# Optimization experiments

Hardware: AMD Instinct MI355X
Metric: run time of the kernel (lower is better)

## Reference

```python
import jax, jax.numpy as jnp
import numpy as np

BETA = 0.8
THR = 1.0  # snntorch Leaky default threshold


def _heaviside(x):
    return (x > 0).astype(x.dtype)


def setup_inputs() -> dict:
    key = jax.random.key(0)
    ks = jax.random.split(key, 8)
    B, T, F, H, L, O = 256, 512, 8, 256, 4, 8
    x = jax.random.normal(ks[0], (B, T, F), dtype=jnp.float32)
    hidden_states = jnp.zeros((B, T, L, H), dtype=jnp.float32)
    prev_obs = jnp.zeros((B, T, F), dtype=jnp.float32)
    readout_states = jnp.zeros((B, T, O), dtype=jnp.float32)
    # fc1: Linear(8, H)
    W1 = jax.random.normal(ks[1], (F, H), dtype=jnp.float32) / np.sqrt(F)
    b1 = jnp.zeros((H,), dtype=jnp.float32)
    # hidden linears: L-1 of [H,H]; final linear [H,O]
    Wh = jax.random.normal(ks[2], (L - 1, H, H), dtype=jnp.float32) / np.sqrt(H)
    bh = jnp.zeros((L - 1, H), dtype=jnp.float32)
    Wout = jax.random.normal(ks[3], (H, O), dtype=jnp.float32) / np.sqrt(H)
    bout = jnp.zeros((O,), dtype=jnp.float32)
    return {"x": x, "hidden_states": hidden_states, "prev_obs": prev_obs,
            "readout_states": readout_states, "W1": W1, "b1": b1,
            "Wh": Wh, "bh": bh, "Wout": Wout, "bout": bout}


def reference(x, hidden_states, prev_obs, readout_states, W1, b1, Wh, bh, Wout, bout):
    # x: [B,T,F]; hidden_states: [B,T,L,H]; readout_states: [B,T,O]
    L = Wh.shape[0] + 1
    mem0 = hidden_states[:, 0]          # [B,L,H]
    ro0 = readout_states[:, 0]          # [B,O]
    # fc1 applied to all timesteps at once (as in the original)
    all_cur = jnp.einsum('btf,fh->bth', x, W1) + b1  # [B,T,H]

    def step(carry, cur_t):
        mem, ro = carry                 # mem: [B,L,H], ro: [B,O]
        cur = cur_t                     # [B,H]
        for i in range(L):
            m = mem[:, i]
            # snntorch Leaky (reset_mechanism='subtract'):
            # reset computed from previous mem, detached
            reset = _heaviside(m - THR)
            m = BETA * m + cur - reset * THR
            spk = _heaviside(m - THR)
            mem = mem.at[:, i].set(m)
            if i < L - 1:
                cur = spk @ Wh[i] + bh[i]
            else:
                cur = spk @ Wout + bout  # [B,O]
        # readout Leaky with reset_mechanism='none'
        ro = BETA * ro + cur
        return (mem, ro), (ro, mem)

    (_, _), (ros, mems) = jax.lax.scan(step, (mem0, ro0), jnp.swapaxes(all_cur, 0, 1))
    outputs = jnp.swapaxes(ros, 0, 1)            # [B,T,O]
    new_hidden_states = jnp.swapaxes(mems, 0, 1)  # [B,T,L,H]
    new_prev_obs = x
    new_readout_states = outputs
    return outputs, new_hidden_states, new_prev_obs, new_readout_states
```

## Files before the change

kernel.cpp:

```cpp
#include <hip/hip_runtime.h>

#define BB   256
#define TT   512
#define FF   8
#define HH   256
#define LL   4
#define OO   8
#define BETA 0.8f
#define THRV 1.0f

#define OFF_OUT  0
#define OFF_HID  (BB*TT*OO)
#define OFF_PREV (OFF_HID + (size_t)BB*TT*LL*HH)
#define OFF_RO   (OFF_PREV + BB*TT*FF)

typedef float nf4 __attribute__((ext_vector_type(4)));

__launch_bounds__(512, 1)
__global__ void snn_kernel(const float* __restrict__ x,
                           const float* __restrict__ hidden_in,
                           const float* __restrict__ readout_in,
                           const float* __restrict__ W1,
                           const float* __restrict__ b1,
                           const float* __restrict__ Wh,
                           const float* __restrict__ bh,
                           const float* __restrict__ Wout,
                           const float* __restrict__ bout,
                           float* __restrict__ out)
{
    __shared__ int   s_list[HH];
    __shared__ int   s_wcnt[4];
    __shared__ float s_part[HH];
    __shared__ float s_rop[4 * OO];

    const int tid  = threadIdx.x;
    const int b    = blockIdx.x;
    const int h    = tid & (HH - 1);
    const int half = tid >> 8;
    const int lane = tid & 63;
    const int wave = tid >> 6;

    {
        const nf4* xs = (const nf4*)(x + (size_t)b * TT * FF);
        nf4*       po = (nf4*)(out + OFF_PREV + (size_t)b * TT * FF);
        #pragma unroll
        for (int i = 0; i < (TT * FF / 4) / 512; ++i)
            __builtin_nontemporal_store(xs[tid + i * 512], po + tid + i * 512);
    }

    float m[LL] = {0, 0, 0, 0};
    float w1c[FF];
    float b1c = 0, bhc0 = 0, bhc1 = 0, bhc2 = 0;
    float wo[OO];
    #pragma unroll
    for (int o = 0; o < OO; ++o) wo[o] = 0.0f;
    if (half == 0) {
        const size_t hb = (size_t)b * TT * LL * HH;
        #pragma unroll
        for (int i = 0; i < LL; ++i) m[i] = hidden_in[hb + i * HH + h];
        #pragma unroll
        for (int f = 0; f < FF; ++f) w1c[f] = W1[f * HH + h];
        b1c  = b1[h];
        bhc0 = bh[0 * HH + h]; bhc1 = bh[1 * HH + h]; bhc2 = bh[2 * HH + h];
        #pragma unroll
        for (int o = 0; o < OO; ++o) wo[o] = Wout[h * OO + o];
    }
    float ro = 0, boutc = 0;
    if (tid < OO) { ro = readout_in[(size_t)b * TT * OO + tid]; boutc = bout[tid]; }

    const float* xb     = x + (size_t)b * TT * FF;
    float* hid_out      = out + OFF_HID + (size_t)b * TT * LL * HH;
    float* out_o        = out + OFF_OUT + (size_t)b * TT * OO;
    float* out_r        = out + OFF_RO  + (size_t)b * TT * OO;

    for (int t = 0; t < TT; ++t) {
        float* hrow = hid_out + (size_t)t * LL * HH;
        float c = 0.0f;
        if (half == 0) {
            c = b1c;
            #pragma unroll
            for (int f = 0; f < FF; ++f) c += xb[t * FF + f] * w1c[f];
        }

        #pragma unroll
        for (int i = 0; i < 3; ++i) {
            int spk = 0;
            unsigned long long bmask = 0ull;
            if (half == 0) {
                float mm = m[i];
                float reset = (mm > THRV) ? THRV : 0.0f;
                mm = BETA * mm + c - reset;
                spk = (mm > THRV) ? 1 : 0;
                m[i] = mm;
                __builtin_nontemporal_store(mm, hrow + i * HH + h);
                bmask = __ballot(spk);
                if (lane == 0) s_wcnt[wave] = __popcll(bmask);
            }
            __syncthreads();
            const int n0 = s_wcnt[0], n1 = s_wcnt[1], n2 = s_wcnt[2], n3 = s_wcnt[3];
            const int n = n0 + n1 + n2 + n3;
            if (half == 0 && spk) {
                int base = (wave > 0 ? n0 : 0) + (wave > 1 ? n1 : 0) + (wave > 2 ? n2 : 0);
                int pos = base + __popcll(bmask & ((1ull << lane) - 1ull));
                s_list[pos] = h << 8;
            }
            __syncthreads();

            const float* Wb = Wh + i * (HH * HH) + h;
            float cc = (half == 0) ? (i == 0 ? bhc0 : (i == 1 ? bhc1 : bhc2)) : 0.0f;
            int j = half;
            while (j + 14 < n) {
                int a0 = s_list[j],      a1 = s_list[j + 2];
                int a2 = s_list[j + 4],  a3 = s_list[j + 6];
                int a4 = s_list[j + 8],  a5 = s_list[j + 10];
                int a6 = s_list[j + 12], a7 = s_list[j + 14];
                float w0 = Wb[a0], w1 = Wb[a1], w2 = Wb[a2], w3 = Wb[a3];
                float w4 = Wb[a4], w5 = Wb[a5], w6 = Wb[a6], w7 = Wb[a7];
                cc += ((w0 + w1) + (w2 + w3)) + ((w4 + w5) + (w6 + w7));
                j += 16;
            }
            while (j < n) { cc += Wb[s_list[j]]; j += 2; }

            if (half == 1) s_part[h] = cc;
            __syncthreads();
            if (half == 0) c = cc + s_part[h];
        }

        if (half == 0) {
            float mm = m[3];
            float reset = (mm > THRV) ? THRV : 0.0f;
            mm = BETA * mm + c - reset;
            int spk3 = (mm > THRV) ? 1 : 0;
            m[3] = mm;
            __builtin_nontemporal_store(mm, hrow + 3 * HH + h);

            float s = spk3 ? 1.0f : 0.0f;
            float c8[OO];
            #pragma unroll
            for (int o = 0; o < OO; ++o) c8[o] = s * wo[o];
            #pragma unroll
            for (int d = 1; d < 64; d <<= 1) {
                #pragma unroll
                for (int o = 0; o < OO; ++o) c8[o] += __shfl_xor(c8[o], d);
            }
            if (lane == 0) {
                #pragma unroll
                for (int o = 0; o < OO; ++o) s_rop[wave * OO + o] = c8[o];
            }
        }
        __syncthreads();
        if (tid < OO) {
            float s = boutc + s_rop[tid] + s_rop[OO + tid] + s_rop[2 * OO + tid] + s_rop[3 * OO + tid];
            ro = BETA * ro + s;
            __builtin_nontemporal_store(ro, out_o + t * OO + tid);
            __builtin_nontemporal_store(ro, out_r + t * OO + tid);
        }
    }
}

extern "C" void kernel_launch(void* const* d_in, const int* in_sizes, int n_in,
                              void* d_out, int out_size, void* d_ws, size_t ws_size,
                              hipStream_t stream) {
    const float* x       = (const float*)d_in[0];
    const float* hidden  = (const float*)d_in[1];
    const float* readout = (const float*)d_in[3];
    const float* W1      = (const float*)d_in[4];
    const float* b1      = (const float*)d_in[5];
    const float* Wh      = (const float*)d_in[6];
    const float* bh      = (const float*)d_in[7];
    const float* Wout    = (const float*)d_in[8];
    const float* bout    = (const float*)d_in[9];
    float* out = (float*)d_out;

    snn_kernel<<<dim3(BB), dim3(512), 0, stream>>>(
        x, hidden, readout, W1, b1, Wh, bh, Wout, bout, out);
}
```

Measured before the change: 2.257 ms.

## Restructure SNN step to cut barriers with atomic spike lists and readout wave

Each layer's spike list is now built with one per-wave atomicAdd into a triple-buffered shared list, replacing the count-then-prefix pass. This reduces the barriers per timestep from about ten to four. The second half of the block, which split the sparse gather, is dropped. A fifth wave computes the Wout readout from the previous step's spike mask, overlapping it with the next step's layers, and the next x row is prefetched. The atomic ordering makes the spike list order nondeterministic, so float summation order varies, and the gather loop also loses the two-way split of work.

Result: faster. 1.899 ms (-15.8%).

```diff
diff --git a/kernel.cpp b/kernel.cpp
--- a/kernel.cpp
+++ b/kernel.cpp
@@ -16,7 +16,56 @@
 
 typedef float nf4 __attribute__((ext_vector_type(4)));
 
-__launch_bounds__(512, 1)
+__device__ __forceinline__ float scan_sum(const int* lst, int n, const float* __restrict__ Wb)
+{
+    float cc = 0.f;
+    int j = 0;
+    if (n >= 8) {
+        int4 e0 = *(const int4*)(lst);
+        int4 e1 = *(const int4*)(lst + 4);
+        float w0 = Wb[e0.x], w1 = Wb[e0.y], w2 = Wb[e0.z], w3 = Wb[e0.w];
+        float w4 = Wb[e1.x], w5 = Wb[e1.y], w6 = Wb[e1.z], w7 = Wb[e1.w];
+        j = 8;
+        while (j + 7 < n) {
+            int4 f0 = *(const int4*)(lst + j);
+            int4 f1 = *(const int4*)(lst + j + 4);
+            float v0 = Wb[f0.x], v1 = Wb[f0.y], v2 = Wb[f0.z], v3 = Wb[f0.w];
+            float v4 = Wb[f1.x], v5 = Wb[f1.y], v6 = Wb[f1.z], v7 = Wb[f1.w];
+            cc += ((w0 + w1) + (w2 + w3)) + ((w4 + w5) + (w6 + w7));
+            w0 = v0; w1 = v1; w2 = v2; w3 = v3;
+            w4 = v4; w5 = v5; w6 = v6; w7 = v7;
+            j += 8;
+        }
+        cc += ((w0 + w1) + (w2 + w3)) + ((w4 + w5) + (w6 + w7));
+    }
+    if (j < n) {
+        int4 e0 = *(const int4*)(lst + j);
+        int4 e1 = *(const int4*)(lst + j + 4);
+        float w0 = Wb[e0.x], w1 = Wb[e0.y], w2 = Wb[e0.z], w3 = Wb[e0.w];
+        float w4 = Wb[e1.x], w5 = Wb[e1.y], w6 = Wb[e1.z], w7 = Wb[e1.w];
+        cc += (j + 0 < n ? w0 : 0.f) + (j + 1 < n ? w1 : 0.f)
+            + (j + 2 < n ? w2 : 0.f) + (j + 3 < n ? w3 : 0.f)
+            + (j + 4 < n ? w4 : 0.f) + (j + 5 < n ? w5 : 0.f)
+            + (j + 6 < n ? w6 : 0.f) + (j + 7 < n ? w7 : 0.f);
+    }
+    return cc;
+}
+
+#define UPDATE_PUBLISH(mreg, li, cval)                                          \
+    {                                                                           \
+        float reset_ = ((mreg) > THRV) ? THRV : 0.f;                            \
+        (mreg) = BETA * (mreg) + (cval) - reset_;                               \
+        int spk_ = ((mreg) > THRV) ? 1 : 0;                                     \
+        __builtin_nontemporal_store((mreg), hrow + (li) * HH + h);              \
+        unsigned long long bm_ = __ballot(spk_);                                \
+        int base_ = 0;                                                          \
+        if (lane == 0) base_ = atomicAdd(&s_total[li], __popcll(bm_));          \
+        base_ = __shfl(base_, 0);                                               \
+        if (spk_)                                                               \
+            s_list[li][base_ + __popcll(bm_ & ((1ull << lane) - 1ull))] = h << 8;\
+    }
+
+__launch_bounds__(320, 1)
 __global__ void snn_kernel(const float* __restrict__ x,
                            const float* __restrict__ hidden_in,
                            const float* __restrict__ readout_in,
@@ -28,132 +77,138 @@
                            const float* __restrict__ bout,
                            float* __restrict__ out)
 {
-    __shared__ int   s_list[HH];
-    __shared__ int   s_wcnt[4];
-    __shared__ float s_part[HH];
-    __shared__ float s_rop[4 * OO];
+    __shared__ int                s_list[3][264];
+    __shared__ int                s_total[3];
+    __shared__ unsigned long long s_mask3[4];
 
     const int tid  = threadIdx.x;
     const int b    = blockIdx.x;
-    const int h    = tid & (HH - 1);
-    const int half = tid >> 8;
     const int lane = tid & 63;
     const int wave = tid >> 6;
+    const int h    = tid & (HH - 1);
+
+    for (int i = tid; i < 3 * 264; i += 320) ((int*)s_list)[i] = 0;
+    if (tid < 3) s_total[tid] = 0;
+    if (tid < 4) s_mask3[tid] = 0ull;
 
     {
         const nf4* xs = (const nf4*)(x + (size_t)b * TT * FF);
         nf4*       po = (nf4*)(out + OFF_PREV + (size_t)b * TT * FF);
-        #pragma unroll
-        for (int i = 0; i < (TT * FF / 4) / 512; ++i)
-            __builtin_nontemporal_store(xs[tid + i * 512], po + tid + i * 512);
-    }
-
-    float m[LL] = {0, 0, 0, 0};
+        for (int i = tid; i < (TT * FF) / 4; i += 320)
+            __builtin_nontemporal_store(xs[i], po + i);
+    }
+
+    float m0 = 0, m1 = 0, m2 = 0, m3 = 0;
     float w1c[FF];
     float b1c = 0, bhc0 = 0, bhc1 = 0, bhc2 = 0;
-    float wo[OO];
-    #pragma unroll
-    for (int o = 0; o < OO; ++o) wo[o] = 0.0f;
-    if (half == 0) {
+    if (tid < 256) {
         const size_t hb = (size_t)b * TT * LL * HH;
-        #pragma unroll
-        for (int i = 0; i < LL; ++i) m[i] = hidden_in[hb + i * HH + h];
+        m0 = hidden_in[hb + 0 * HH + h];
+        m1 = hidden_in[hb + 1 * HH + h];
+        m2 = hidden_in[hb + 2 * HH + h];
+        m3 = hidden_in[hb + 3 * HH + h];
         #pragma unroll
         for (int f = 0; f < FF; ++f) w1c[f] = W1[f * HH + h];
         b1c  = b1[h];
         bhc0 = bh[0 * HH + h]; bhc1 = bh[1 * HH + h]; bhc2 = bh[2 * HH + h];
-        #pragma unroll
-        for (int o = 0; o < OO; ++o) wo[o] = Wout[h * OO + o];
-    }
-    float ro = 0, boutc = 0;
-    if (tid < OO) { ro = readout_in[(size_t)b * TT * OO + tid]; boutc = bout[tid]; }
-
-    const float* xb     = x + (size_t)b * TT * FF;
-    float* hid_out      = out + OFF_HID + (size_t)b * TT * LL * HH;
-    float* out_o        = out + OFF_OUT + (size_t)b * TT * OO;
-    float* out_r        = out + OFF_RO  + (size_t)b * TT * OO;
-
+    }
+
+    const int o8  = lane & 7;
+    const int seg = lane >> 3;
+    float ro = 0.f, boutc = 0.f;
+    if (wave == 4 && lane < 8) {
+        ro    = readout_in[(size_t)b * TT * OO + lane];
+        boutc = bout[lane];
+    }
+
+    const float* xb  = x + (size_t)b * TT * FF;
+    const float* Wb0 = Wh + h;
+    const float* Wb1 = Wh + 1 * HH * HH + h;
+    const float* Wb2 = Wh + 2 * HH * HH + h;
+    float* hid_out = out + OFF_HID + (size_t)b * TT * LL * HH;
+    float* out_o   = out + OFF_OUT + (size_t)b * TT * OO;
+    float* out_r   = out + OFF_RO  + (size_t)b * TT * OO;
+
+    nf4 xv0 = {0, 0, 0, 0}, xv1 = {0, 0, 0, 0};
+    if (tid < 256) { xv0 = ((const nf4*)xb)[0]; xv1 = ((const nf4*)xb)[1]; }
+
+    __syncthreads();
+
+    #pragma unroll 1
     for (int t = 0; t < TT; ++t) {
         float* hrow = hid_out + (size_t)t * LL * HH;
-        float c = 0.0f;
-        if (half == 0) {
-            c = b1c;
-            #pragma unroll
-            for (int f = 0; f < FF; ++f) c += xb[t * FF + f] * w1c[f];
-        }
-
-        #pragma unroll
-        for (int i = 0; i < 3; ++i) {
-            int spk = 0;
-            unsigned long long bmask = 0ull;
-            if (half == 0) {
-                float mm = m[i];
-                float reset = (mm > THRV) ? THRV : 0.0f;
-                mm = BETA * mm + c - reset;
-                spk = (mm > THRV) ? 1 : 0;
-                m[i] = mm;
-                __builtin_nontemporal_store(mm, hrow + i * HH + h);
-                bmask = __ballot(spk);
-                if (lane == 0) s_wcnt[wave] = __popcll(bmask);
+
+        if (tid < 256) {
+            float c = b1c + xv0.x * w1c[0] + xv0.y * w1c[1] + xv0.z * w1c[2] + xv0.w * w1c[3]
+                          + xv1.x * w1c[4] + xv1.y * w1c[5] + xv1.z * w1c[6] + xv1.w * w1c[7];
+            UPDATE_PUBLISH(m0, 0, c);
+        } else if (tid == 256) {
+            s_total[2] = 0;
+        }
+        __syncthreads();
+
+        if (tid < 256) {
+            const int tn = (t + 1 < TT) ? t + 1 : t;
+            xv0 = ((const nf4*)(xb + tn * FF))[0];
+            xv1 = ((const nf4*)(xb + tn * FF))[1];
+            float c = bhc0 + scan_sum(s_list[0], s_total[0], Wb0);
+            UPDATE_PUBLISH(m1, 1, c);
+        } else if (t > 0) {
+            unsigned sm = ((const unsigned*)s_mask3)[seg];
+            float acc = 0.f;
+            while (sm) {
+                int r = __builtin_ctz(sm);
+                sm &= sm - 1;
+                acc += Wout[((seg << 5) + r) * OO + o8];
             }
-            __syncthreads();
-            const int n0 = s_wcnt[0], n1 = s_wcnt[1], n2 = s_wcnt[2], n3 = s_wcnt[3];
-            const int n = n0 + n1 + n2 + n3;
-            if (half == 0 && spk) {
-                int base = (wave > 0 ? n0 : 0) + (wave > 1 ? n1 : 0) + (wave > 2 ? n2 : 0);
-                int pos = base + __popcll(bmask & ((1ull << lane) - 1ull));
-                s_list[pos] = h << 8;
+            acc += __shfl_xor(acc, 8);
+            acc += __shfl_xor(acc, 16);
+            acc += __shfl_xor(acc, 32);
+            if (lane < 8) {
+                ro = BETA * ro + (acc + boutc);
+                __builtin_nontemporal_store(ro, out_o + (t - 1) * OO + lane);
+                __builtin_nontemporal_store(ro, out_r + (t - 1) * OO + lane);
             }
-            __syncthreads();
-
-            const float* Wb = Wh + i * (HH * HH) + h;
-            float cc = (half == 0) ? (i == 0 ? bhc0 : (i == 1 ? bhc1 : bhc2)) : 0.0f;
-            int j = half;
-            while (j + 14 < n) {
-                int a0 = s_list[j],      a1 = s_list[j + 2];
-                int a2 = s_list[j + 4],  a3 = s_list[j + 6];
-                int a4 = s_list[j + 8],  a5 = s_list[j + 10];
-                int a6 = s_list[j + 12], a7 = s_list[j + 14];
-                float w0 = Wb[a0], w1 = Wb[a1], w2 = Wb[a2], w3 = Wb[a3];
-                float w4 = Wb[a4], w5 = Wb[a5], w6 = Wb[a6], w7 = Wb[a7];
-                cc += ((w0 + w1) + (w2 + w3)) + ((w4 + w5) + (w6 + w7));
-                j += 16;
-            }
-            while (j < n) { cc += Wb[s_list[j]]; j += 2; }
-
-            if (half == 1) s_part[h] = cc;
-            __syncthreads();
-            if (half == 0) c = cc + s_part[h];
-        }
-
-        if (half == 0) {
-            float mm = m[3];
-            float reset = (mm > THRV) ? THRV : 0.0f;
-            mm = BETA * mm + c - reset;
-            int spk3 = (mm > THRV) ? 1 : 0;
-            m[3] = mm;
-            __builtin_nontemporal_store(mm, hrow + 3 * HH + h);
-
-            float s = spk3 ? 1.0f : 0.0f;
-            float c8[OO];
-            #pragma unroll
-            for (int o = 0; o < OO; ++o) c8[o] = s * wo[o];
-            #pragma unroll
-            for (int d = 1; d < 64; d <<= 1) {
-                #pragma unroll
-                for (int o = 0; o < OO; ++o) c8[o] += __shfl_xor(c8[o], d);
-            }
-            if (lane == 0) {
-                #pragma unroll
-                for (int o = 0; o < OO; ++o) s_rop[wave * OO + o] = c8[o];
-            }
-        }
-        __syncthreads();
-        if (tid < OO) {
-            float s = boutc + s_rop[tid] + s_rop[OO + tid] + s_rop[2 * OO + tid] + s_rop[3 * OO + tid];
-            ro = BETA * ro + s;
-            __builtin_nontemporal_store(ro, out_o + t * OO + tid);
-            __builtin_nontemporal_store(ro, out_r + t * OO + tid);
+        }
+        __syncthreads();
+
+        if (tid < 256) {
+            float c = bhc1 + scan_sum(s_list[1], s_total[1], Wb1);
+            UPDATE_PUBLISH(m2, 2, c);
+        } else if (tid == 256) {
+            s_total[0] = 0;
+        }
+        __syncthreads();
+
+        if (tid < 256) {
+            float c = bhc2 + scan_sum(s_list[2], s_total[2], Wb2);
+            float reset_ = (m3 > THRV) ? THRV : 0.f;
+            m3 = BETA * m3 + c - reset_;
+            int spk_ = (m3 > THRV) ? 1 : 0;
+            __builtin_nontemporal_store(m3, hrow + 3 * HH + h);
+            unsigned long long bm_ = __ballot(spk_);
+            if (lane == 0) s_mask3[wave] = bm_;
+        } else if (tid == 256) {
+            s_total[1] = 0;
+        }
+        __syncthreads();
+    }
+
+    if (wave == 4) {
+        unsigned sm = ((const unsigned*)s_mask3)[seg];
+        float acc = 0.f;
+        while (sm) {
+            int r = __builtin_ctz(sm);
+            sm &= sm - 1;
+            acc += Wout[((seg << 5) + r) * OO + o8];
+        }
+        acc += __shfl_xor(acc, 8);
+        acc += __shfl_xor(acc, 16);
+        acc += __shfl_xor(acc, 32);
+        if (lane < 8) {
+            ro = BETA * ro + (acc + boutc);
+            __builtin_nontemporal_store(ro, out_o + (TT - 1) * OO + lane);
+            __builtin_nontemporal_store(ro, out_r + (TT - 1) * OO + lane);
         }
     }
 }
@@ -172,6 +227,6 @@
     const float* bout    = (const float*)d_in[9];
     float* out = (float*)d_out;
 
-    snn_kernel<<<dim3(BB), dim3(512), 0, stream>>>(
+    snn_kernel<<<dim3(BB), dim3(320), 0, stream>>>(
         x, hidden, readout, W1, b1, Wh, bh, Wout, bout, out);
 }
```
